# Performance work log

Hardware: AMD Instinct MI355X
Metric: run time of the kernel (lower is better)

The kernel has to match this reference:

```python
import jax, jax.numpy as jnp
import numpy as np

# Static configuration (uniform ragged layout: every sequence has the same lengths)
B = 8          # number of sequences
QLEN = 256     # new query tokens per sequence
D = 1024       # embedding_dim
H = 16         # num_attention_heads
HD = D // H    # head dim = 64
FFN = 4096     # ffn_embedding_dim
PAGE = 16      # KV-cache page size
KV_TOTAL = 4096            # total KV length per sequence (prefix + new)
P = KV_TOTAL // PAGE       # pages per sequence = 256
NEW_PAGES = QLEN // PAGE   # pages occupied by the new tokens = 16
NUM_PAGES = B * P          # 2048
PREFIX = KV_TOTAL - QLEN   # cached prefix length per sequence
SCALE = HD ** -0.5
LN_EPS = 1e-5


def layer_norm(x, g, b):
    mu = jnp.mean(x, axis=-1, keepdims=True)
    var = jnp.mean(jnp.square(x - mu), axis=-1, keepdims=True)
    return (x - mu) * jax.lax.rsqrt(var + LN_EPS) * g + b


def setup_inputs() -> dict:
    key = jax.random.key(0)
    ks = jax.random.split(key, 12)
    s = 0.02
    inp = {
        "x": jax.random.normal(ks[0], (B * QLEN, D), jnp.float32),
        "pagetable": jax.random.normal(ks[1], (NUM_PAGES, 2, PAGE, H, HD), jnp.float32) * 0.5,
        "Wq": jax.random.normal(ks[2], (D, D), jnp.float32) * s,
        "bq": jnp.zeros((D,), jnp.float32),
        "Wk": jax.random.normal(ks[3], (D, D), jnp.float32) * s,
        "bk": jnp.zeros((D,), jnp.float32),
        "Wv": jax.random.normal(ks[4], (D, D), jnp.float32) * s,
        "bv": jnp.zeros((D,), jnp.float32),
        "Wo": jax.random.normal(ks[5], (D, D), jnp.float32) * s,
        "bo": jnp.zeros((D,), jnp.float32),
        "ln1_g": jnp.ones((D,), jnp.float32),
        "ln1_b": jnp.zeros((D,), jnp.float32),
        "W1": jax.random.normal(ks[6], (D, FFN), jnp.float32) * s,
        "b1": jnp.zeros((FFN,), jnp.float32),
        "W2": jax.random.normal(ks[7], (FFN, D), jnp.float32) * s,
        "b2": jnp.zeros((D,), jnp.float32),
        "lnf_g": jnp.ones((D,), jnp.float32),
        "lnf_b": jnp.zeros((D,), jnp.float32),
        "qo_indptr": jnp.arange(B + 1, dtype=jnp.int32) * QLEN,
        "paged_kv_indptr": jnp.arange(B + 1, dtype=jnp.int32) * P,
        "paged_kv_indices": jnp.arange(NUM_PAGES, dtype=jnp.int32),
        "paged_kv_last_page_len": jnp.full((B,), PAGE, jnp.int32),
        "layer_idx": 0,
    }
    return inp


def reference(x, pagetable, Wq, bq, Wk, bk, Wv, bv, Wo, bo,
              ln1_g, ln1_b, W1, b1, W2, b2, lnf_g, lnf_b,
              qo_indptr, paged_kv_indptr, paged_kv_indices,
              paged_kv_last_page_len, layer_idx):
    residual = x

    # ---- paged self-attention (post-LN path: layer_norm_first=False) ----
    q = ((x @ Wq + bq) * SCALE).reshape(B, QLEN, H, HD)
    k_new = (x @ Wk + bk).reshape(B, QLEN, H, HD)
    v_new = (x @ Wv + bv).reshape(B, QLEN, H, HD)

    # append new K/V into the last NEW_PAGES pages of each sequence
    page_ids = paged_kv_indices.reshape(B, P)                 # [B, P]
    new_ids = page_ids[:, P - NEW_PAGES:].reshape(-1)         # [B*NEW_PAGES]
    kv_new = jnp.stack([k_new, v_new], axis=2)                # [B, QLEN, 2, H, HD]
    kv_new = kv_new.reshape(B, NEW_PAGES, PAGE, 2, H, HD).transpose(0, 1, 3, 2, 4, 5)
    pt = pagetable.at[new_ids].set(kv_new.reshape(-1, 2, PAGE, H, HD))

    # gather the full paged KV per sequence
    kv = pt[page_ids]                                         # [B, P, 2, PAGE, H, HD]
    K = kv[:, :, 0].reshape(B, KV_TOTAL, H, HD)
    V = kv[:, :, 1].reshape(B, KV_TOTAL, H, HD)

    # streaming-causal mask: query i attends to kv positions <= PREFIX + i
    scores = jnp.einsum("bqhd,bkhd->bhqk", q, K)              # [B, H, QLEN, KV_TOTAL]
    kv_pos = jnp.arange(KV_TOTAL)[None, :]
    q_pos = PREFIX + jnp.arange(QLEN)[:, None]
    scores = jnp.where(kv_pos <= q_pos, scores, jnp.float32(-1e30))
    attn = jax.nn.softmax(scores, axis=-1)
    ctx = jnp.einsum("bhqk,bkhd->bqhd", attn, V).reshape(B * QLEN, D)
    x = ctx @ Wo + bo

    x = residual + x
    x = layer_norm(x, ln1_g, ln1_b)

    # ---- FFN ----
    residual = x
    x = jax.nn.relu(x @ W1 + b1)
    x = x @ W2 + b2
    layer_result = x
    x = residual + x
    x = layer_norm(x, lnf_g, lnf_b)

    return x, layer_result, pt
```

## Files before the change

kernel.cpp:

```cpp
#include <hip/hip_runtime.h>
#include <hip/hip_bf16.h>

typedef unsigned short u16;
typedef __attribute__((ext_vector_type(4))) float f32x4;
typedef __attribute__((ext_vector_type(8))) short short8;

#define MODE_QKV 0
#define MODE_WO  1
#define MODE_F1  2
#define MODE_F2  3

__device__ inline u16 f2bf(float f) {
    __hip_bfloat16 h = __float2bfloat16(f);
    return *(u16*)&h;
}
__device__ inline float bf2f(u16 u) {
    union { unsigned int i; float f; } x; x.i = ((unsigned int)u) << 16; return x.f;
}

typedef __attribute__((address_space(3))) unsigned int lds_u32_t;
typedef const __attribute__((address_space(1))) unsigned int glb_u32_t;
__device__ inline void gload16(const u16* g, u16* l) {
    __builtin_amdgcn_global_load_lds((glb_u32_t*)(const void*)g,
                                     (lds_u32_t*)(void*)l, 16, 0, 0);
}

__global__ __launch_bounds__(256) void prep_wx(
    const float* __restrict__ Wq, const float* __restrict__ Wk,
    const float* __restrict__ Wv, const float* __restrict__ x,
    u16* __restrict__ WqkvT, u16* __restrict__ xb) {
    int bid = blockIdx.x;
    int tid = threadIdx.x;
    int tx = tid & 31, ty = tid >> 5;
    if (bid >= 3072) {
        int i = (bid - 3072) * 256 + tid;
        const float4* p = (const float4*)(x + (size_t)i * 8);
        float4 a = p[0], b = p[1];
        u16 t[8] = {f2bf(a.x), f2bf(a.y), f2bf(a.z), f2bf(a.w),
                    f2bf(b.x), f2bf(b.y), f2bf(b.z), f2bf(b.w)};
        *(uint4*)(xb + (size_t)i * 8) = *(const uint4*)t;
        return;
    }
    int m = bid >> 10, r = bid & 1023;
    const float* src = (m == 0) ? Wq : (m == 1) ? Wk : Wv;
    u16* dst = WqkvT + (size_t)m * 1024 * 1024;
    __shared__ float t[32][33];
    int n0 = (r & 31) * 32, k0 = (r >> 5) * 32;
#pragma unroll
    for (int j = 0; j < 32; j += 8)
        t[ty + j][tx] = src[(size_t)(k0 + ty + j) * 1024 + n0 + tx];
    __syncthreads();
#pragma unroll
    for (int j = 0; j < 32; j += 8)
        dst[(size_t)(n0 + ty + j) * 1024 + k0 + tx] = f2bf(t[tx][ty + j]);
}

__global__ __launch_bounds__(256) void ln_wo(const float* __restrict__ p0,
                                             const float* __restrict__ p1,
                                             const float* __restrict__ bo,
                                             const float* __restrict__ resid,
                                             const float* __restrict__ g,
                                             const float* __restrict__ be,
                                             float* __restrict__ outf,
                                             u16* __restrict__ outb) {
    int row = blockIdx.x;
    int tid = threadIdx.x;
    int c = tid * 4;
    size_t o = (size_t)row * 1024 + c;
    f32x4 v = *(const f32x4*)(p0 + o) + *(const f32x4*)(p1 + o)
            + *(const f32x4*)(bo + c) + *(const f32x4*)(resid + o);
    float s = v[0] + v[1] + v[2] + v[3];
#pragma unroll
    for (int m = 1; m < 64; m <<= 1) s += __shfl_xor(s, m, 64);
    __shared__ float red1[4], red2[4];
    int w = tid >> 6;
    if ((tid & 63) == 0) red1[w] = s;
    __syncthreads();
    float mu = (red1[0] + red1[1] + red1[2] + red1[3]) * (1.0f / 1024.0f);
    f32x4 d = v - mu;
    float q = d[0] * d[0] + d[1] * d[1] + d[2] * d[2] + d[3] * d[3];
#pragma unroll
    for (int m = 1; m < 64; m <<= 1) q += __shfl_xor(q, m, 64);
    if ((tid & 63) == 0) red2[w] = q;
    __syncthreads();
    float var = (red2[0] + red2[1] + red2[2] + red2[3]) * (1.0f / 1024.0f);
    float rs = rsqrtf(var + 1e-5f);
    f32x4 gg = *(const f32x4*)(g + c), bb = *(const f32x4*)(be + c);
    f32x4 ov = d * rs * gg + bb;
    *(f32x4*)(outf + o) = ov;
    u16 t[4] = {f2bf(ov[0]), f2bf(ov[1]), f2bf(ov[2]), f2bf(ov[3])};
    *(uint2*)&outb[o] = *(const uint2*)t;
}

__global__ __launch_bounds__(256) void ln_f2(const float* __restrict__ q0,
                                             const float* __restrict__ b2,
                                             const float* __restrict__ xln1f,
                                             const float* __restrict__ g,
                                             const float* __restrict__ be,
                                             float* __restrict__ out_lr,
                                             float* __restrict__ out_x) {
    int row = blockIdx.x;
    int tid = threadIdx.x;
    int c = tid * 4;
    size_t o = (size_t)row * 1024 + c;
    const size_t st = (size_t)2048 * 1024;
    f32x4 v = *(const f32x4*)(q0 + o) + *(const f32x4*)(q0 + st + o)
            + *(const f32x4*)(q0 + 2 * st + o) + *(const f32x4*)(q0 + 3 * st + o)
            + *(const f32x4*)(b2 + c);
    *(f32x4*)(out_lr + o) = v;
    v = v + *(const f32x4*)(xln1f + o);
    float s = v[0] + v[1] + v[2] + v[3];
#pragma unroll
    for (int m = 1; m < 64; m <<= 1) s += __shfl_xor(s, m, 64);
    __shared__ float red1[4], red2[4];
    int w = tid >> 6;
    if ((tid & 63) == 0) red1[w] = s;
    __syncthreads();
    float mu = (red1[0] + red1[1] + red1[2] + red1[3]) * (1.0f / 1024.0f);
    f32x4 d = v - mu;
    float q = d[0] * d[0] + d[1] * d[1] + d[2] * d[2] + d[3] * d[3];
#pragma unroll
    for (int m = 1; m < 64; m <<= 1) q += __shfl_xor(q, m, 64);
    if ((tid & 63) == 0) red2[w] = q;
    __syncthreads();
    float var = (red2[0] + red2[1] + red2[2] + red2[3]) * (1.0f / 1024.0f);
    float rs = rsqrtf(var + 1e-5f);
    f32x4 gg = *(const f32x4*)(g + c), bb = *(const f32x4*)(be + c);
    *(f32x4*)(out_x + o) = d * rs * gg + bb;
}

template <int MODE>
__device__ __forceinline__ void gemm_body(
    u16* As, u16* Bs, int m0, int n0,
    const u16* __restrict__ A, const u16* __restrict__ Bt, int lda, int Kspan, int N,
    const float* __restrict__ bias0, const float* __restrict__ bias1,
    const float* __restrict__ bias2,
    float* __restrict__ o0, u16* __restrict__ ob,
    u16* __restrict__ kbf, u16* __restrict__ vbf, const int* __restrict__ kvidx) {
    int tid = threadIdx.x;
    int l = tid & 63, w = tid >> 6;
    int wr = w >> 1, wc = w & 1;
    int lr = l & 15, lg = l >> 4;
    int lrow8 = l >> 3;
    int scol = ((l & 7) ^ lrow8) << 3;
    f32x4 acc[4][4] = {};
    for (int kb = 0; kb < Kspan; kb += 64) {
#pragma unroll
        for (int p = 0; p < 4; ++p) {
            int chunk = p * 4 + w;
            int r = chunk * 8 + lrow8;
            gload16(&A[(size_t)(m0 + r) * lda + kb + scol], &As[chunk * 512]);
            gload16(&Bt[(size_t)(n0 + r) * lda + kb + scol], &Bs[chunk * 512]);
        }
        __syncthreads();
#pragma unroll
        for (int kk = 0; kk < 2; ++kk) {
            short8 a[4], b[4];
            int c0 = kk * 32 + lg * 8;
#pragma unroll
            for (int mi = 0; mi < 4; mi++) {
                int row = wr * 64 + mi * 16 + lr;
                a[mi] = *(const short8*)&As[row * 64 + (c0 ^ ((row & 7) << 3))];
            }
#pragma unroll
            for (int ni = 0; ni < 4; ni++) {
                int row = wc * 64 + ni * 16 + lr;
                b[ni] = *(const short8*)&Bs[row * 64 + (c0 ^ ((row & 7) << 3))];
            }
#pragma unroll
            for (int mi = 0; mi < 4; mi++)
#pragma unroll
                for (int ni = 0; ni < 4; ni++)
                    acc[mi][ni] = __builtin_amdgcn_mfma_f32_16x16x32_bf16(
                        a[mi], b[ni], acc[mi][ni], 0, 0, 0);
        }
        __syncthreads();
    }
#pragma unroll
    for (int mi = 0; mi < 4; mi++) {
#pragma unroll
        for (int ni = 0; ni < 4; ni++) {
#pragma unroll
            for (int r = 0; r < 4; r++) {
                int row = m0 + wr * 64 + mi * 16 + lg * 4 + r;
                int col = n0 + wc * 64 + ni * 16 + lr;
                float v = acc[mi][ni][r];
                if constexpr (MODE == MODE_QKV) {
                    int sel = col >> 10, c = col & 1023;
                    int b = row >> 8, ii = row & 255;
                    int h = (c >> 6), hd = c & 63;
                    if (sel == 0) {
                        ob[(size_t)row * 1024 + c] = f2bf((v + bias0[c]) * 0.125f);
                    } else if (sel == 1) {
                        float val = v + bias1[c];
                        int page = kvidx[b * 256 + 240 + (ii >> 4)];
                        o0[(size_t)page * 32768 + (size_t)(ii & 15) * 1024 + c] = val;
                        kbf[((size_t)(b * 16 + h) * 4096 + 3840 + ii) * 64 + hd] = f2bf(val);
                    } else {
                        float val = v + bias2[c];
                        int page = kvidx[b * 256 + 240 + (ii >> 4)];
                        o0[(size_t)page * 32768 + 16384 + (size_t)(ii & 15) * 1024 + c] = val;
                        vbf[((size_t)(b * 16 + h) * 64 + hd) * 4096 + 3840 + ii] = f2bf(val);
                    }
                } else if constexpr (MODE == MODE_F1) {
                    float t = v + bias0[col];
                    ob[(size_t)row * N + col] = f2bf(fmaxf(t, 0.0f));
                } else {
                    o0[(size_t)row * N + col] = v;
                }
            }
        }
    }
}

template <int MODE>
__global__ __launch_bounds__(256) void gemm_nt(
    const u16* __restrict__ A, const u16* __restrict__ Bt,
    int lda, int Kspan, int N, int gx, int nper,
    const float* __restrict__ bias0,
    float* __restrict__ o0, u16* __restrict__ ob, size_t osplit) {
    __shared__ __align__(16) u16 smem[128 * 64 * 2];
    int bid = blockIdx.x;
    int split = bid / nper, t = bid % nper;
    gemm_body<MODE>(smem, smem + 128 * 64, (t / gx) * 128, (t % gx) * 128,
                    A + (size_t)split * Kspan, Bt + (size_t)split * Kspan,
                    lda, Kspan, N, bias0, nullptr, nullptr,
                    o0 ? o0 + (size_t)split * osplit : nullptr, ob,
                    nullptr, nullptr, nullptr);
}

__global__ __launch_bounds__(256) void mega_prep(
    const u16* __restrict__ xb, const u16* __restrict__ WqkvT,
    const float* __restrict__ bq, const float* __restrict__ bk,
    const float* __restrict__ bv,
    float* __restrict__ out_pt, u16* __restrict__ qbuf,
    u16* __restrict__ Kbf, u16* __restrict__ Vtbf,
    const float* __restrict__ pgt, const int* __restrict__ kvidx) {
    __shared__ __align__(16) u16 smem[128 * 64 * 2];
    int bid = blockIdx.x;
    int tid = threadIdx.x;
    if (bid < 384) {
        gemm_body<MODE_QKV>(smem, smem + 8192, (bid / 24) * 128, (bid % 24) * 128,
                            xb, WqkvT, 1024, 1024, 3072, bq, bk, bv,
                            out_pt, qbuf, Kbf, Vtbf, kvidx);
        return;
    }
    if (bid < 1344) {
        int idx = (bid - 384) * 2;
#pragma unroll
        for (int pp = 0; pp < 2; ++pp) {
            int p = idx + pp;
            int b = p / 240, slot = p % 240;
            int page = kvidx[b * 256 + slot];
            const float4* s = (const float4*)(pgt + (size_t)page * 32768);
            float4* d = (float4*)(out_pt + (size_t)page * 32768);
#pragma unroll 8
            for (int it = 0; it < 32; ++it) d[it * 256 + tid] = s[it * 256 + tid];
        }
        return;
    }
    if (bid < 1824) {
        int idx = bid - 1344;
        int tile = idx % 60, b = idx / 60;
        int T0 = tile * 64;
        int h = tid >> 4, hd0 = (tid & 15) * 4;
        int pg[4];
#pragma unroll
        for (int pi = 0; pi < 4; ++pi) pg[pi] = kvidx[b * 256 + (T0 >> 4) + pi];
#pragma unroll 4
        for (int it2 = 0; it2 < 64; ++it2) {
            int pi = it2 >> 4, it = it2 & 15;
            const float* src = pgt + (size_t)pg[pi] * 32768;
            size_t o = (size_t)it * 1024 + tid * 4;
            float4 f = *(const float4*)(src + o);
            u16 k4[4] = {f2bf(f.x), f2bf(f.y), f2bf(f.z), f2bf(f.w)};
            size_t kdst = ((size_t)(b * 16 + h) * 4096 + T0 + pi * 16 + it) * 64 + hd0;
            *(uint2*)&Kbf[kdst] = *(const uint2*)k4;
        }
        return;
    }
    int vb2 = bid - 1824;
    int tile = vb2 % 60, b = vb2 / 60;
    int T0 = tile * 64;
    int pg[4];
#pragma unroll
    for (int pi = 0; pi < 4; ++pi) pg[pi] = kvidx[b * 256 + (T0 >> 4) + pi];
    u16* vt = smem;
    for (int hb2 = 0; hb2 < 8; ++hb2) {
#pragma unroll 4
        for (int it = 0; it < 8; ++it) {
            int ti = it * 8 + (tid >> 5);
            int pi = ti >> 4, tokloc = ti & 15;
            int c4 = (tid & 31) * 4;
            size_t o = (size_t)pg[pi] * 32768 + 16384 + (size_t)tokloc * 1024
                       + hb2 * 128 + c4;
            float4 v = *(const float4*)(pgt + o);
            u16 v4[4] = {f2bf(v.x), f2bf(v.y), f2bf(v.z), f2bf(v.w)};
            *(uint2*)&vt[ti * 134 + c4] = *(const uint2*)v4;
        }
        __syncthreads();
        int g = tid >> 4, j = tid & 15;
#pragma unroll
        for (int rp = 0; rp < 8; ++rp) {
            int ri = rp * 16 + g;
            int h = hb2 * 2 + (ri >> 6), hd = ri & 63;
            u16 o4[4];
#pragma unroll
            for (int s = 0; s < 4; ++s) o4[s] = vt[(j * 4 + s) * 134 + ri];
            *(uint2*)&Vtbf[((size_t)(b * 16 + h) * 64 + hd) * 4096 + T0 + j * 4] =
                *(const uint2*)o4;
        }
        __syncthreads();
    }
}

__global__ __launch_bounds__(512) void attn_kernel(const u16* __restrict__ qb,
                                                   const u16* __restrict__ Kbf,
                                                   const u16* __restrict__ Vtbf,
                                                   u16* __restrict__ pOct,
                                                   float* __restrict__ pL,
                                                   const float* __restrict__ Wo,
                                                   const float* __restrict__ W1,
                                                   const float* __restrict__ W2,
                                                   u16* __restrict__ WoT,
                                                   u16* __restrict__ W1T,
                                                   u16* __restrict__ W2T) {
    __shared__ u16 Ks[64 * 64];
    __shared__ u16 Vt[64 * 64];
    __shared__ u16 Ps[8][16 * 64];
    int bid = blockIdx.x;
    int tid = threadIdx.x;
    if (bid >= 1024) {
        int sub = tid >> 8, t2 = tid & 255;
        int wb = (bid - 1024) * 2 + sub;
        const float* src; u16* dst; int K, N, bx, by;
        if (wb < 1024) {
            bx = wb & 31; by = wb >> 5; K = 1024; N = 1024; src = Wo; dst = WoT;
        } else if (wb < 5120) {
            int r = wb - 1024; bx = r & 127; by = r >> 7; K = 1024; N = 4096; src = W1; dst = W1T;
        } else {
            int r = wb - 5120; bx = r & 31; by = r >> 5; K = 4096; N = 1024; src = W2; dst = W2T;
        }
        float* t = sub ? (float*)Vt : (float*)Ks;
        int tx = t2 & 31, ty = t2 >> 5;
        int n0 = bx * 32, k0 = by * 32;
#pragma unroll
        for (int jj = 0; jj < 32; jj += 8)
            t[(ty + jj) * 33 + tx] = src[(size_t)(k0 + ty + jj) * N + n0 + tx];
        __syncthreads();
#pragma unroll
        for (int jj = 0; jj < 32; jj += 8)
            dst[(size_t)(n0 + ty + jj) * K + k0 + tx] = f2bf(t[tx * 33 + ty + jj]);
        return;
    }
    int l = tid & 63, w = tid >> 6;
    int lr = l & 15, lg = l >> 4;
    int x = bid & 7, qt = x >> 2, split = x & 3;
    int h = (bid >> 3) & 15, b = bid >> 7;

    int qrow = qt * 128 + w * 16 + lr;
    const u16* qptr = qb + (size_t)(b * 256 + qrow) * 1024 + h * 64 + lg * 8;
    short8 qf0 = *(const short8*)qptr;
    short8 qf1 = *(const short8*)(qptr + 32);

    const u16* kslab = Kbf + (size_t)(b * 16 + h) * 4096 * 64;
    const u16* vslab = Vtbf + (size_t)(b * 16 + h) * 64 * 4096;

    f32x4 octx[4] = {};
    f32x4 lacc = {};
    short8 ones;
#pragma unroll
    for (int jj = 0; jj < 8; jj++) ones[jj] = (short)0x3F80;

    int qbase = 3840 + qt * 128;
    int ntiles = (qbase + 128) >> 6;
    int tstart = split * 16;
    int tend = min(tstart + 16, ntiles);
    int kt0 = tstart * 64, kt1 = tend * 64;

    int srow = tid >> 3, scol8 = (tid & 7) * 8;
    int sdst = srow * 64 + (scol8 ^ ((srow & 7) << 3));
    const u16* kp = kslab + srow * 64 + scol8;
    const u16* vp = vslab + (size_t)srow * 4096 + scol8;

    uint4 kreg = *(const uint4*)(kp + (size_t)kt0 * 64);
    uint4 vreg = *(const uint4*)(vp + kt0);
    for (int kt = kt0; kt < kt1; kt += 64) {
        *(uint4*)&Ks[sdst] = kreg;
        *(uint4*)&Vt[sdst] = vreg;
        __syncthreads();
        bool hn = (kt + 64) < kt1;
        if (hn) {
            kreg = *(const uint4*)(kp + (size_t)(kt + 64) * 64);
            vreg = *(const uint4*)(vp + kt + 64);
        }
        float P[4][4];
        bool need_mask = (kt + 63 > qbase);
        __builtin_amdgcn_s_setprio(1);
#pragma unroll
        for (int ni = 0; ni < 4; ni++) {
            f32x4 s = {};
            int krow = ni * 16 + lr;
            int swz = (krow & 7) << 3;
            short8 k0 = *(const short8*)&Ks[krow * 64 + ((lg * 8) ^ swz)];
            short8 k1 = *(const short8*)&Ks[krow * 64 + ((32 + lg * 8) ^ swz)];
            s = __builtin_amdgcn_mfma_f32_16x16x32_bf16(qf0, k0, s, 0, 0, 0);
            s = __builtin_amdgcn_mfma_f32_16x16x32_bf16(qf1, k1, s, 0, 0, 0);
            if (need_mask) {
                int col = kt + ni * 16 + lr;
#pragma unroll
                for (int r = 0; r < 4; r++) {
                    int q = qt * 128 + w * 16 + lg * 4 + r;
                    P[ni][r] = (col <= 3840 + q) ? __expf(s[r]) : 0.0f;
                }
            } else {
#pragma unroll
                for (int r = 0; r < 4; r++) P[ni][r] = __expf(s[r]);
            }
        }
        __builtin_amdgcn_s_setprio(0);
#pragma unroll
        for (int ni = 0; ni < 4; ni++)
#pragma unroll
            for (int r = 0; r < 4; r++) {
                int prow = lg * 4 + r;
                Ps[w][prow * 64 + ((ni * 16 + lr) ^ ((prow & 7) << 3))] = f2bf(P[ni][r]);
            }
        __builtin_amdgcn_s_setprio(1);
#pragma unroll
        for (int kk = 0; kk < 2; kk++) {
            int c0 = kk * 32 + lg * 8;
            short8 pf = *(const short8*)&Ps[w][lr * 64 + (c0 ^ ((lr & 7) << 3))];
            lacc = __builtin_amdgcn_mfma_f32_16x16x32_bf16(pf, ones, lacc, 0, 0, 0);
#pragma unroll
            for (int dt = 0; dt < 4; dt++) {
                int vrow = dt * 16 + lr;
                short8 vf = *(const short8*)&Vt[vrow * 64 + (c0 ^ ((vrow & 7) << 3))];
                octx[dt] = __builtin_amdgcn_mfma_f32_16x16x32_bf16(pf, vf, octx[dt], 0, 0, 0);
            }
        }
        __builtin_amdgcn_s_setprio(0);
        __syncthreads();
    }
    size_t obase = (((size_t)(split * 8 + b) * 16 + h) * 256 + qt * 128) * 64;
#pragma unroll
    for (int dt = 0; dt < 4; dt++)
#pragma unroll
        for (int r = 0; r < 4; r++)
            pOct[obase + (size_t)(w * 16 + lg * 4 + r) * 64 + dt * 16 + lr] =
                f2bf(octx[dt][r]);
    if (lr == 0) {
        size_t lbase = ((size_t)(split * 8 + b) * 16 + h) * 256 + qt * 128;
#pragma unroll
        for (int r = 0; r < 4; r++) pL[lbase + w * 16 + lg * 4 + r] = lacc[r];
    }
}

__global__ __launch_bounds__(256) void attn_combine(const u16* __restrict__ pOct,
                                                    const float* __restrict__ pL,
                                                    u16* __restrict__ ctxb) {
    int row = blockIdx.x;
    int b = row >> 8, q = row & 255;
    int tid = threadIdx.x;
    int h = tid >> 4, dq = (tid & 15) * 4;
    size_t stride = (size_t)128 * 256 * 64;
    size_t base = ((size_t)(b * 16 + h) * 256 + q) * 64 + dq;
    size_t lstride = 128 * 256;
    size_t lbase = (size_t)(b * 16 + h) * 256 + q;
    f32x4 s = {};
    float ls = 0.0f;
#pragma unroll
    for (int sp = 0; sp < 4; sp++) {
        u16 a[4];
        *(uint2*)a = *(const uint2*)&pOct[sp * stride + base];
#pragma unroll
        for (int j = 0; j < 4; j++) s[j] += bf2f(a[j]);
        ls += pL[sp * lstride + lbase];
    }
    float inv = 1.0f / ls;
    u16 o[4] = {f2bf(s[0] * inv), f2bf(s[1] * inv), f2bf(s[2] * inv), f2bf(s[3] * inv)};
    *(uint2*)&ctxb[(size_t)row * 1024 + h * 64 + dq] = *(const uint2*)o;
}

extern "C" void kernel_launch(void* const* d_in, const int* in_sizes, int n_in,
                              void* d_out, int out_size, void* d_ws, size_t ws_size,
                              hipStream_t stream) {
    (void)in_sizes; (void)n_in; (void)out_size; (void)ws_size;
    const float* x   = (const float*)d_in[0];
    const float* pgt = (const float*)d_in[1];
    const float* Wq  = (const float*)d_in[2];
    const float* bq  = (const float*)d_in[3];
    const float* Wk  = (const float*)d_in[4];
    const float* bk  = (const float*)d_in[5];
    const float* Wv  = (const float*)d_in[6];
    const float* bv  = (const float*)d_in[7];
    const float* Wo  = (const float*)d_in[8];
    const float* bo  = (const float*)d_in[9];
    const float* ln1g = (const float*)d_in[10];
    const float* ln1b = (const float*)d_in[11];
    const float* W1  = (const float*)d_in[12];
    const float* b1  = (const float*)d_in[13];
    const float* W2  = (const float*)d_in[14];
    const float* b2  = (const float*)d_in[15];
    const float* lnfg = (const float*)d_in[16];
    const float* lnfb = (const float*)d_in[17];
    const int* kvidx = (const int*)d_in[20];

    float* out = (float*)d_out;
    float* out_x  = out;
    float* out_lr = out + 2048 * 1024;
    float* out_pt = out + 2 * 2048 * 1024;

    char* ws = (char*)d_ws;
    size_t off = 0;
    auto alloc = [&](size_t bytes) { void* p = ws + off; off += (bytes + 255) & ~(size_t)255; return p; };
    u16* WqkvT = (u16*)alloc((size_t)3072 * 1024 * 2);
    u16* WoT   = (u16*)alloc((size_t)1024 * 1024 * 2);
    u16* W1T   = (u16*)alloc((size_t)4096 * 1024 * 2);
    u16* W2T   = (u16*)alloc((size_t)1024 * 4096 * 2);
    u16* xb    = (u16*)alloc((size_t)2048 * 1024 * 2);
    u16* qbuf  = (u16*)alloc((size_t)2048 * 1024 * 2);
    u16* ctxb  = (u16*)alloc((size_t)2048 * 1024 * 2);
    char* regB = (char*)alloc((size_t)168 * 1024 * 1024);
    u16* Kbf  = (u16*)regB;
    u16* Vtbf = (u16*)(regB + (size_t)64 * 1024 * 1024);
    u16*   pOct = (u16*)(regB + (size_t)128 * 1024 * 1024);
    float* pL   = (float*)(regB + (size_t)162 * 1024 * 1024);
    float* p0    = (float*)regB;
    float* xln1f = (float*)(regB + (size_t)16 * 1024 * 1024);
    u16*   xln1b = (u16*)(regB + (size_t)24 * 1024 * 1024);
    u16*   hb    = (u16*)(regB + (size_t)32 * 1024 * 1024);
    float* q0    = (float*)(regB + (size_t)128 * 1024 * 1024);

    prep_wx<<<4096, 256, 0, stream>>>(Wq, Wk, Wv, x, WqkvT, xb);
    mega_prep<<<2304, 256, 0, stream>>>(xb, WqkvT, bq, bk, bv,
                                        out_pt, qbuf, Kbf, Vtbf, pgt, kvidx);
    attn_kernel<<<5632, 512, 0, stream>>>(qbuf, Kbf, Vtbf, pOct, pL,
                                          Wo, W1, W2, WoT, W1T, W2T);
    attn_combine<<<2048, 256, 0, stream>>>(pOct, pL, ctxb);
    gemm_nt<MODE_WO><<<256, 256, 0, stream>>>(ctxb, WoT, 1024, 512, 1024, 8, 128,
        nullptr, p0, nullptr, (size_t)2048 * 1024);
    ln_wo<<<2048, 256, 0, stream>>>(p0, p0 + (size_t)2048 * 1024, bo, x,
                                    ln1g, ln1b, xln1f, xln1b);
    gemm_nt<MODE_F1><<<512, 256, 0, stream>>>(xln1b, W1T, 1024, 1024, 4096, 32, 512,
        b1, nullptr, hb, 0);
    gemm_nt<MODE_F2><<<512, 256, 0, stream>>>(hb, W2T, 4096, 1024, 1024, 8, 128,
        nullptr, q0, nullptr, (size_t)2048 * 1024);
    ln_f2<<<2048, 256, 0, stream>>>(q0, b2, xln1f, lnfg, lnfb, out_lr, out_x);
}
```

Before: 353.2 us.

## Fuse prefix page copy with K/V bf16 conversion and interleave GEMM blocks

The prefix-page copy, K conversion and V transpose were separate block ranges in the prep kernel. They are merged into one per-(batch, head, 64-token tile) block that reads each K/V element once, writes the fp32 copy to the output page table, and writes the bf16 K and transposed V. The QKV GEMM tiles are spread through the grid (one in every 21 blocks) so they overlap with the memory-bound copy work. This removes a second read of the prefix pages but uses many more, smaller blocks whose 256-byte row segments may coalesce less well.

```diff
diff --git a/kernel.cpp b/kernel.cpp
--- a/kernel.cpp
+++ b/kernel.cpp
@@ -239,78 +239,44 @@
     __shared__ __align__(16) u16 smem[128 * 64 * 2];
     int bid = blockIdx.x;
     int tid = threadIdx.x;
-    if (bid < 384) {
-        gemm_body<MODE_QKV>(smem, smem + 8192, (bid / 24) * 128, (bid % 24) * 128,
+    if (bid % 21 == 20) {
+        int t = bid / 21;
+        gemm_body<MODE_QKV>(smem, smem + 8192, (t / 24) * 128, (t % 24) * 128,
                             xb, WqkvT, 1024, 1024, 3072, bq, bk, bv,
                             out_pt, qbuf, Kbf, Vtbf, kvidx);
         return;
     }
-    if (bid < 1344) {
-        int idx = (bid - 384) * 2;
-#pragma unroll
-        for (int pp = 0; pp < 2; ++pp) {
-            int p = idx + pp;
-            int b = p / 240, slot = p % 240;
-            int page = kvidx[b * 256 + slot];
-            const float4* s = (const float4*)(pgt + (size_t)page * 32768);
-            float4* d = (float4*)(out_pt + (size_t)page * 32768);
-#pragma unroll 8
-            for (int it = 0; it < 32; ++it) d[it * 256 + tid] = s[it * 256 + tid];
-        }
-        return;
-    }
-    if (bid < 1824) {
-        int idx = bid - 1344;
-        int tile = idx % 60, b = idx / 60;
-        int T0 = tile * 64;
-        int h = tid >> 4, hd0 = (tid & 15) * 4;
-        int pg[4];
-#pragma unroll
-        for (int pi = 0; pi < 4; ++pi) pg[pi] = kvidx[b * 256 + (T0 >> 4) + pi];
-#pragma unroll 4
-        for (int it2 = 0; it2 < 64; ++it2) {
-            int pi = it2 >> 4, it = it2 & 15;
-            const float* src = pgt + (size_t)pg[pi] * 32768;
-            size_t o = (size_t)it * 1024 + tid * 4;
-            float4 f = *(const float4*)(src + o);
-            u16 k4[4] = {f2bf(f.x), f2bf(f.y), f2bf(f.z), f2bf(f.w)};
-            size_t kdst = ((size_t)(b * 16 + h) * 4096 + T0 + pi * 16 + it) * 64 + hd0;
-            *(uint2*)&Kbf[kdst] = *(const uint2*)k4;
-        }
-        return;
-    }
-    int vb2 = bid - 1824;
-    int tile = vb2 % 60, b = vb2 / 60;
+    int idx = (bid / 21) * 20 + (bid % 21);
+    int tile = idx % 60, rest = idx / 60;
+    int h = rest & 15, b = rest >> 4;
     int T0 = tile * 64;
-    int pg[4];
-#pragma unroll
-    for (int pi = 0; pi < 4; ++pi) pg[pi] = kvidx[b * 256 + (T0 >> 4) + pi];
+    int rr = tid >> 4;
+    int hdq = tid & 15;
     u16* vt = smem;
-    for (int hb2 = 0; hb2 < 8; ++hb2) {
-#pragma unroll 4
-        for (int it = 0; it < 8; ++it) {
-            int ti = it * 8 + (tid >> 5);
-            int pi = ti >> 4, tokloc = ti & 15;
-            int c4 = (tid & 31) * 4;
-            size_t o = (size_t)pg[pi] * 32768 + 16384 + (size_t)tokloc * 1024
-                       + hb2 * 128 + c4;
-            float4 v = *(const float4*)(pgt + o);
-            u16 v4[4] = {f2bf(v.x), f2bf(v.y), f2bf(v.z), f2bf(v.w)};
-            *(uint2*)&vt[ti * 134 + c4] = *(const uint2*)v4;
-        }
-        __syncthreads();
-        int g = tid >> 4, j = tid & 15;
-#pragma unroll
-        for (int rp = 0; rp < 8; ++rp) {
-            int ri = rp * 16 + g;
-            int h = hb2 * 2 + (ri >> 6), hd = ri & 63;
-            u16 o4[4];
-#pragma unroll
-            for (int s = 0; s < 4; ++s) o4[s] = vt[(j * 4 + s) * 134 + ri];
-            *(uint2*)&Vtbf[((size_t)(b * 16 + h) * 64 + hd) * 4096 + T0 + j * 4] =
-                *(const uint2*)o4;
-        }
-        __syncthreads();
+    size_t kdst_base = ((size_t)(b * 16 + h) * 4096 + T0) * 64;
+#pragma unroll
+    for (int p = 0; p < 4; ++p) {
+        int i = p * 16 + rr;
+        int page = kvidx[b * 256 + (T0 >> 4) + p];
+        size_t src = (size_t)page * 32768 + (size_t)rr * 1024 + h * 64 + hdq * 4;
+        float4 kf = *(const float4*)(pgt + src);
+        *(float4*)(out_pt + src) = kf;
+        u16 kb4[4] = {f2bf(kf.x), f2bf(kf.y), f2bf(kf.z), f2bf(kf.w)};
+        *(uint2*)&Kbf[kdst_base + (size_t)i * 64 + hdq * 4] = *(const uint2*)kb4;
+        float4 vf = *(const float4*)(pgt + src + 16384);
+        *(float4*)(out_pt + src + 16384) = vf;
+        u16 vb4[4] = {f2bf(vf.x), f2bf(vf.y), f2bf(vf.z), f2bf(vf.w)};
+        *(uint2*)&vt[i * 68 + hdq * 4] = *(const uint2*)vb4;
+    }
+    __syncthreads();
+    size_t vdst_base = (size_t)(b * 16 + h) * 64 * 4096 + T0;
+#pragma unroll
+    for (int p = 0; p < 4; ++p) {
+        int hd = p * 16 + rr;
+        u16 o[4];
+#pragma unroll
+        for (int j = 0; j < 4; ++j) o[j] = vt[(hdq * 4 + j) * 68 + hd];
+        *(uint2*)&Vtbf[vdst_base + (size_t)hd * 4096 + hdq * 4] = *(const uint2*)o;
     }
 }
 
@@ -533,7 +499,7 @@
     float* q0    = (float*)(regB + (size_t)128 * 1024 * 1024);
 
     prep_wx<<<4096, 256, 0, stream>>>(Wq, Wk, Wv, x, WqkvT, xb);
-    mega_prep<<<2304, 256, 0, stream>>>(xb, WqkvT, bq, bk, bv,
+    mega_prep<<<8064, 256, 0, stream>>>(xb, WqkvT, bq, bk, bv,
                                         out_pt, qbuf, Kbf, Vtbf, pgt, kvidx);
     attn_kernel<<<5632, 512, 0, stream>>>(qbuf, Kbf, Vtbf, pOct, pL,
                                           Wo, W1, W2, WoT, W1T, W2T);
```

Result: faster. 328.0 us (-7.1%).
